# Performance work log

Hardware: AMD Instinct MI355X
Metric: run time of the kernel (lower is better)

Reference implementation:

```python
import jax, jax.numpy as jnp
import numpy as np

N_NODES = 50000
N_EDGES = 400000
N_GRAPHS = 500
N_FEAT = 4
EMB = 200
HID = 128


def setup_inputs() -> dict:
    key = jax.random.key(0)
    ks = jax.random.split(key, 16)
    x = jax.random.normal(ks[0], (N_NODES, N_FEAT), dtype=jnp.float32)
    edge_index = jax.random.randint(ks[1], (2, N_EDGES), 0, N_NODES, dtype=jnp.int64)
    x_scalar = jax.random.normal(ks[2], (N_GRAPHS, N_FEAT), dtype=jnp.float32)
    batch_index = jnp.sort(jax.random.randint(ks[3], (N_NODES,), 0, N_GRAPHS, dtype=jnp.int64))

    def lin(k, fan_in, fan_out):
        return jax.random.normal(k, (fan_in, fan_out), dtype=jnp.float32) / np.sqrt(fan_in)

    params = {
        'W0': lin(ks[4], N_FEAT, EMB), 'b0': jnp.zeros((EMB,), jnp.float32),
        'W1': lin(ks[5], EMB, EMB), 'b1': jnp.zeros((EMB,), jnp.float32),
        'W2': lin(ks[6], EMB, EMB), 'b2': jnp.zeros((EMB,), jnp.float32),
        'W3': lin(ks[7], EMB, EMB), 'b3': jnp.zeros((EMB,), jnp.float32),
        'Wl1': lin(ks[8], EMB + N_FEAT, HID),
        'bl1': jax.random.normal(ks[9], (HID,), jnp.float32) * 0.01,
        'Wl2': lin(ks[10], HID, 1),
        'bl2': jax.random.normal(ks[11], (1,), jnp.float32) * 0.01,
    }
    return dict(x=x, edge_index=edge_index, x_scalar=x_scalar, batch_index=batch_index, **params)


def _gcn_conv(h, W, b, src, dst, norm, num_nodes):
    # PyG GCNConv: h' = D^-1/2 (A+I) D^-1/2 (h W) + b, with precomputed edge norms
    m = (h @ W)[src] * norm[:, None]            # [E+N, out]
    out = jax.ops.segment_sum(m, dst, num_segments=num_nodes)
    return out + b


def reference(x, edge_index, x_scalar, batch_index,
              W0, b0, W1, b1, W2, b2, W3, b3, Wl1, bl1, Wl2, bl2):
    num_nodes = x.shape[0]
    loops = jnp.arange(num_nodes, dtype=edge_index.dtype)
    src = jnp.concatenate([edge_index[0], loops])  # self-loops appended
    dst = jnp.concatenate([edge_index[1], loops])
    deg = jax.ops.segment_sum(jnp.ones_like(dst, dtype=x.dtype), dst, num_segments=num_nodes)
    dinv = deg ** -0.5                              # deg >= 1 due to self-loops
    norm = dinv[src] * dinv[dst]

    h = jax.nn.leaky_relu(_gcn_conv(x, W0, b0, src, dst, norm, num_nodes), 0.01)
    h = jax.nn.leaky_relu(_gcn_conv(h, W1, b1, src, dst, norm, num_nodes), 0.01)
    h = jax.nn.leaky_relu(_gcn_conv(h, W2, b2, src, dst, norm, num_nodes), 0.01)
    h = jax.nn.leaky_relu(_gcn_conv(h, W3, b3, src, dst, norm, num_nodes), 0.01)

    # global mean pool per graph
    sums = jax.ops.segment_sum(h, batch_index, num_segments=N_GRAPHS)
    cnt = jax.ops.segment_sum(jnp.ones((num_nodes,), h.dtype), batch_index, num_segments=N_GRAPHS)
    pooled = sums / jnp.maximum(cnt, 1.0)[:, None]

    g = jnp.concatenate([pooled, x_scalar], axis=1)   # [G, EMB+4]
    g = jax.nn.leaky_relu(g @ Wl1 + bl1, 0.01)
    out = g @ Wl2 + bl2                                # [G, 1]
    return out
```

## Files before the change

kernel.cpp:

```cpp
#include <hip/hip_runtime.h>
#include <math.h>

#define LEAKY(v) ((v) > 0.0f ? (v) : 0.01f * (v))

typedef _Float16 v8h __attribute__((ext_vector_type(8)));
typedef float v4f __attribute__((ext_vector_type(4)));

__global__ void k_count(const int* __restrict__ ei, int* __restrict__ cnt, int E) {
    int e = blockIdx.x * blockDim.x + threadIdx.x;
    if (e < E) atomicAdd(&cnt[ei[E + e]], 1);
}

__global__ __launch_bounds__(256) void k_scan1(const int* __restrict__ cnt,
                                               int* __restrict__ rowptr,
                                               int* __restrict__ bsum, int n) {
    __shared__ int s[256];
    int t = threadIdx.x, i = blockIdx.x * 256 + t;
    int v = (i < n) ? cnt[i] : 0;
    s[t] = v;
    __syncthreads();
    for (int off = 1; off < 256; off <<= 1) {
        int u = (t >= off) ? s[t - off] : 0;
        __syncthreads();
        s[t] += u;
        __syncthreads();
    }
    if (i < n) rowptr[i] = s[t] - v;
    if (t == 255) bsum[blockIdx.x] = s[255];
}

__global__ __launch_bounds__(256) void k_scan2(int* __restrict__ bsum, int nb) {
    __shared__ int s[256];
    int t = threadIdx.x;
    int v = (t < nb) ? bsum[t] : 0;
    s[t] = v;
    __syncthreads();
    for (int off = 1; off < 256; off <<= 1) {
        int u = (t >= off) ? s[t - off] : 0;
        __syncthreads();
        s[t] += u;
        __syncthreads();
    }
    if (t < nb) bsum[t] = s[t] - v;
}

__global__ __launch_bounds__(256) void k_scan3(int* __restrict__ rowptr,
                                               const int* __restrict__ bsum,
                                               const int* __restrict__ cnt,
                                               float* __restrict__ dinv, int n,
                                               float* __restrict__ pooled, int npool) {
    int i = blockIdx.x * 256 + threadIdx.x;
    if (i < n) {
        rowptr[i] += bsum[blockIdx.x];
        dinv[i] = rsqrtf(1.0f + (float)cnt[i]);
    }
    for (int j = i; j < npool; j += gridDim.x * 256) pooled[j] = 0.0f;
}

__global__ void k_fill(const int* __restrict__ ei, const float* __restrict__ dinv,
                       int* __restrict__ rowptr, int2* __restrict__ adj, int E) {
    int e = blockIdx.x * blockDim.x + threadIdx.x;
    if (e < E) {
        int s = ei[e], d = ei[E + e];
        int pos = atomicAdd(&rowptr[d], 1);
        adj[pos] = make_int2(s, __float_as_int(dinv[s] * dinv[d]));
    }
}

__global__ __launch_bounds__(256) void k_splitW3(const float* __restrict__ W1,
                                                 const float* __restrict__ W2,
                                                 const float* __restrict__ W3,
                                                 _Float16* __restrict__ th0, _Float16* __restrict__ tl0,
                                                 _Float16* __restrict__ th1, _Float16* __restrict__ tl1,
                                                 _Float16* __restrict__ th2, _Float16* __restrict__ tl2,
                                                 int* __restrict__ cnt, int n) {
    int layer = blockIdx.y;
    const float* W = (layer == 0) ? W1 : (layer == 1) ? W2 : W3;
    _Float16* Wth = (layer == 0) ? th0 : (layer == 1) ? th1 : th2;
    _Float16* Wtl = (layer == 0) ? tl0 : (layer == 1) ? tl1 : tl2;
    int idx = blockIdx.x * blockDim.x + threadIdx.x;
    int gidx = (blockIdx.y * gridDim.x + blockIdx.x) * 256 + threadIdx.x;
    for (int j = gidx; j < n; j += gridDim.x * gridDim.y * 256) cnt[j] = 0;
    if (idx >= 224 * 208) return;
    int k = idx / 208, c = idx - k * 208;
    float v = (k < 200 && c < 200) ? W[k * 200 + c] : 0.0f;
    _Float16 hi = (_Float16)v;
    _Float16 lo = (_Float16)(v - (float)hi);
    Wth[c * 224 + k] = hi;
    Wtl[c * 224 + k] = lo;
}

__global__ __launch_bounds__(256, 4) void k_gemm200_mfma_l0(const float* __restrict__ x,
                                                            const float* __restrict__ dinv,
                                                            const int* __restrict__ rowptr,
                                                            const int2* __restrict__ adj,
                                                            const float* __restrict__ W0,
                                                            const float* __restrict__ b0,
                                                            const _Float16* __restrict__ Wth,
                                                            const _Float16* __restrict__ Wtl,
                                                            _Float16* __restrict__ T, int M) {
    __shared__ _Float16 Wsh[208 * 32];
    __shared__ _Float16 Wsl[208 * 32];
    __shared__ float W0s[4][200];
    __shared__ float b0s[200];
    const int tid  = threadIdx.x;
    const int lane = tid & 63;
    const int wid  = tid >> 6;
    const int quad = lane >> 4;
    const int l16  = lane & 15;
    const int rowA = blockIdx.x * 64 + wid * 16 + l16;
    const int rowAc = min(rowA, M - 1);

    float w0n = dinv[rowAc]; w0n *= w0n;
    float4 xv = ((const float4*)x)[rowAc];
    float4 pxv = make_float4(xv.x * w0n, xv.y * w0n, xv.z * w0n, xv.w * w0n);
    {
        int lo = rowAc ? rowptr[rowAc - 1] : 0;
        int hi = rowptr[rowAc];
        for (int j = lo; j < hi; ++j) {
            int2 cw = adj[j];
            float w = __int_as_float(cw.y);
            float4 sv = ((const float4*)x)[cw.x];
            pxv.x += sv.x * w; pxv.y += sv.y * w; pxv.z += sv.z * w; pxv.w += sv.w * w;
        }
    }

    for (int idx = tid; idx < 1000; idx += 256) {
        if (idx < 800) W0s[idx / 200][idx % 200] = W0[idx];
        else b0s[idx - 800] = b0[idx - 800];
    }
    __syncthreads();

    v4f acc[13];
#pragma unroll
    for (int t = 0; t < 13; ++t) acc[t] = 0.0f;

    for (int k0 = 0; k0 < 224; k0 += 32) {
        v8h ah, al;
        int kb = k0 + quad * 8;
        if (kb < 200) {
#pragma unroll
            for (int j = 0; j < 8; ++j) {
                int k = kb + j;
                float pv = pxv.x * W0s[0][k] + pxv.y * W0s[1][k]
                         + pxv.z * W0s[2][k] + pxv.w * W0s[3][k] + b0s[k];
                pv = LEAKY(pv);
                _Float16 h = (_Float16)pv;
                ah[j] = h;
                al[j] = (_Float16)(pv - (float)h);
            }
        } else {
#pragma unroll
            for (int j = 0; j < 8; ++j) { ah[j] = (_Float16)0.0f; al[j] = (_Float16)0.0f; }
        }
        __syncthreads();
        for (int idx = tid; idx < 832; idx += 256) {
            int nr = idx >> 2, part = idx & 3;
            *(uint4*)&Wsh[nr * 32 + part * 8] = *(const uint4*)&Wth[nr * 224 + k0 + part * 8];
            *(uint4*)&Wsl[nr * 32 + part * 8] = *(const uint4*)&Wtl[nr * 224 + k0 + part * 8];
        }
        __syncthreads();
#pragma unroll
        for (int t = 0; t < 13; ++t) {
            int nidx = (t * 16 + l16) * 32 + quad * 8;
            v8h wh = *(const v8h*)&Wsh[nidx];
            v8h wl = *(const v8h*)&Wsl[nidx];
            acc[t] = __builtin_amdgcn_mfma_f32_16x16x32_f16(ah, wh, acc[t], 0, 0, 0);
            acc[t] = __builtin_amdgcn_mfma_f32_16x16x32_f16(ah, wl, acc[t], 0, 0, 0);
            acc[t] = __builtin_amdgcn_mfma_f32_16x16x32_f16(al, wh, acc[t], 0, 0, 0);
        }
    }
    const int rb = blockIdx.x * 64 + wid * 16 + quad * 4;
#pragma unroll
    for (int t = 0; t < 13; ++t) {
        int c = t * 16 + l16;
        if (c < 200) {
#pragma unroll
            for (int e = 0; e < 4; ++e) {
                int r = rb + e;
                if (r < M) T[(size_t)r * 200 + c] = (_Float16)acc[t][e];
            }
        }
    }
}

__global__ __launch_bounds__(256, 4) void k_gemm200_mfma(const _Float16* __restrict__ P,
                                                         const float* __restrict__ bias,
                                                         const _Float16* __restrict__ Wth,
                                                         const _Float16* __restrict__ Wtl,
                                                         _Float16* __restrict__ T, int M) {
    __shared__ _Float16 Wsh[208 * 32];
    __shared__ _Float16 Wsl[208 * 32];
    const int tid  = threadIdx.x;
    const int lane = tid & 63;
    const int wid  = tid >> 6;
    const int quad = lane >> 4;
    const int l16  = lane & 15;
    const int rowA = blockIdx.x * 64 + wid * 16 + l16;
    const int rowAc = min(rowA, M - 1);
    const _Float16* Prow = P + (size_t)rowAc * 200;

    v4f acc[13];
#pragma unroll
    for (int t = 0; t < 13; ++t) acc[t] = 0.0f;

    for (int k0 = 0; k0 < 224; k0 += 32) {
        v8h ah, al;
        int kb = k0 + quad * 8;
        if (kb < 200) {
            v8h ph = *(const v8h*)(Prow + kb);
            float4 ba = *(const float4*)(bias + kb);
            float4 bb = *(const float4*)(bias + kb + 4);
            float bv[8] = {ba.x, ba.y, ba.z, ba.w, bb.x, bb.y, bb.z, bb.w};
#pragma unroll
            for (int j = 0; j < 8; ++j) {
                float av = (float)ph[j] + bv[j];
                av = LEAKY(av);
                _Float16 h = (_Float16)av;
                ah[j] = h;
                al[j] = (_Float16)(av - (float)h);
            }
        } else {
#pragma unroll
            for (int j = 0; j < 8; ++j) { ah[j] = (_Float16)0.0f; al[j] = (_Float16)0.0f; }
        }
        __syncthreads();
        for (int idx = tid; idx < 832; idx += 256) {
            int nr = idx >> 2, part = idx & 3;
            *(uint4*)&Wsh[nr * 32 + part * 8] = *(const uint4*)&Wth[nr * 224 + k0 + part * 8];
            *(uint4*)&Wsl[nr * 32 + part * 8] = *(const uint4*)&Wtl[nr * 224 + k0 + part * 8];
        }
        __syncthreads();
#pragma unroll
        for (int t = 0; t < 13; ++t) {
            int nidx = (t * 16 + l16) * 32 + quad * 8;
            v8h wh = *(const v8h*)&Wsh[nidx];
            v8h wl = *(const v8h*)&Wsl[nidx];
            acc[t] = __builtin_amdgcn_mfma_f32_16x16x32_f16(ah, wh, acc[t], 0, 0, 0);
            acc[t] = __builtin_amdgcn_mfma_f32_16x16x32_f16(ah, wl, acc[t], 0, 0, 0);
            acc[t] = __builtin_amdgcn_mfma_f32_16x16x32_f16(al, wh, acc[t], 0, 0, 0);
        }
    }
    const int rb = blockIdx.x * 64 + wid * 16 + quad * 4;
#pragma unroll
    for (int t = 0; t < 13; ++t) {
        int c = t * 16 + l16;
        if (c < 200) {
#pragma unroll
            for (int e = 0; e < 4; ++e) {
                int r = rb + e;
                if (r < M) T[(size_t)r * 200 + c] = (_Float16)acc[t][e];
            }
        }
    }
}

__global__ __launch_bounds__(256) void k_gather200h(const _Float16* __restrict__ t,
                                                    const float* __restrict__ dinv,
                                                    const int* __restrict__ rowptr,
                                                    const int2* __restrict__ adj,
                                                    _Float16* __restrict__ p, int n) {
    int gid = blockIdx.x * blockDim.x + threadIdx.x;
    if (gid >= n * 25) return;
    int v = gid / 25, c8 = gid - v * 25;
    const v8h* tp = (const v8h*)t;
    float w0 = dinv[v]; w0 *= w0;
    v8h tv = tp[v * 25 + c8];
    float a0[8], a1[8];
#pragma unroll
    for (int i = 0; i < 8; ++i) { a0[i] = (float)tv[i] * w0; a1[i] = 0.0f; }
    int lo = v ? rowptr[v - 1] : 0;
    int hi = rowptr[v];
    int j = lo;
    for (; j + 1 < hi; j += 2) {
        int2 e0 = adj[j], e1 = adj[j + 1];
        float wa = __int_as_float(e0.y), wb = __int_as_float(e1.y);
        v8h s0 = tp[e0.x * 25 + c8];
        v8h s1 = tp[e1.x * 25 + c8];
#pragma unroll
        for (int i = 0; i < 8; ++i) {
            a0[i] += (float)s0[i] * wa;
            a1[i] += (float)s1[i] * wb;
        }
    }
    if (j < hi) {
        int2 cw = adj[j];
        float w = __int_as_float(cw.y);
        v8h sv = tp[cw.x * 25 + c8];
#pragma unroll
        for (int i = 0; i < 8; ++i) a0[i] += (float)sv[i] * w;
    }
    v8h o;
#pragma unroll
    for (int i = 0; i < 8; ++i) o[i] = (_Float16)(a0[i] + a1[i]);
    ((v8h*)p)[v * 25 + c8] = o;
}

__global__ __launch_bounds__(256) void k_poolsum(const _Float16* __restrict__ p3,
                                                 const float* __restrict__ b3,
                                                 const int* __restrict__ batch, int n,
                                                 float* __restrict__ pooled) {
    int c = threadIdx.x;
    if (c >= 200) return;
    int base = blockIdx.x * 64;
    int end = min(base + 64, n);
    float bc = b3[c];
    int gprev = batch[base];
    float s = 0.0f;
    for (int i = base; i < end; ++i) {
        int g = batch[i];
        float v = (float)p3[(size_t)i * 200 + c] + bc;
        v = LEAKY(v);
        if (g != gprev) {
            atomicAdd(&pooled[gprev * 200 + c], s);
            s = 0.0f;
            gprev = g;
        }
        s += v;
    }
    atomicAdd(&pooled[gprev * 200 + c], s);
}

__global__ __launch_bounds__(128) void k_mlpfin(const float* __restrict__ pooled,
                                                const int* __restrict__ batch, int n_nodes,
                                                const float* __restrict__ xs,
                                                const float* __restrict__ Wl1,
                                                const float* __restrict__ bl1,
                                                const float* __restrict__ Wl2,
                                                const float* __restrict__ bl2,
                                                float* __restrict__ out) {
    __shared__ float grow[204];
    __shared__ float partial[2];
    __shared__ int sb[2];
    int g = blockIdx.x;
    int t = threadIdx.x;
    if (t == 0) {
        int lo = 0, hi = n_nodes;
        while (lo < hi) { int m = (lo + hi) >> 1; if (batch[m] < g) lo = m + 1; else hi = m; }
        sb[0] = lo;
        int lo2 = lo, hi2 = n_nodes;
        while (lo2 < hi2) { int m = (lo2 + hi2) >> 1; if (batch[m] < g + 1) lo2 = m + 1; else hi2 = m; }
        sb[1] = lo2;
    }
    __syncthreads();
    float inv = 1.0f / fmaxf((float)(sb[1] - sb[0]), 1.0f);
    for (int idx = t; idx < 200; idx += 128) grow[idx] = pooled[g * 200 + idx] * inv;
    if (t < 4) grow[200 + t] = xs[g * 4 + t];
    __syncthreads();
    float s = bl1[t];
    for (int k = 0; k < 204; ++k) s += grow[k] * Wl1[k * 128 + t];
    s = LEAKY(s);
    float hv = s * Wl2[t];
    for (int off = 32; off > 0; off >>= 1) hv += __shfl_down(hv, off, 64);
    if ((t & 63) == 0) partial[t >> 6] = hv;
    __syncthreads();
    if (t == 0) out[g] = partial[0] + partial[1] + bl2[0];
}

extern "C" void kernel_launch(void* const* d_in, const int* in_sizes, int n_in,
                              void* d_out, int out_size, void* d_ws, size_t ws_size,
                              hipStream_t stream) {
    const float* x    = (const float*)d_in[0];
    const int*   ei   = (const int*)d_in[1];
    const float* xs   = (const float*)d_in[2];
    const int*   batch= (const int*)d_in[3];
    const float* W0   = (const float*)d_in[4];
    const float* b0   = (const float*)d_in[5];
    const float* W1   = (const float*)d_in[6];
    const float* b1   = (const float*)d_in[7];
    const float* W2   = (const float*)d_in[8];
    const float* b2   = (const float*)d_in[9];
    const float* W3   = (const float*)d_in[10];
    const float* b3   = (const float*)d_in[11];
    const float* Wl1  = (const float*)d_in[12];
    const float* bl1  = (const float*)d_in[13];
    const float* Wl2  = (const float*)d_in[14];
    const float* bl2  = (const float*)d_in[15];
    float* out = (float*)d_out;

    const int N = in_sizes[0] / 4;
    const int E = in_sizes[1] / 2;
    const int G = in_sizes[2] / 4;

    char* ws = (char*)d_ws;
    size_t off = 0;
    auto alloc = [&](size_t bytes) { void* p = ws + off; off += (bytes + 255) & ~size_t(255); return p; };
    _Float16* bufA = (_Float16*)alloc((size_t)N * 200 * sizeof(_Float16));
    _Float16* bufB = (_Float16*)alloc((size_t)N * 200 * sizeof(_Float16));
    float* dinv   = (float*)alloc((size_t)N * sizeof(float));
    float* pooled = (float*)alloc((size_t)G * 200 * sizeof(float));
    int*   cnt    = (int*)alloc((size_t)N * sizeof(int));
    int*   rowptr = (int*)alloc(((size_t)N + 1) * sizeof(int));
    int*   bsum   = (int*)alloc(256 * sizeof(int));
    int2*  adj    = (int2*)alloc((size_t)E * sizeof(int2));
    _Float16* Wth[3]; _Float16* Wtl[3];
    for (int i = 0; i < 3; ++i) {
        Wth[i] = (_Float16*)alloc(208 * 224 * sizeof(_Float16));
        Wtl[i] = (_Float16*)alloc(208 * 224 * sizeof(_Float16));
    }

    const int B = 256;
    const int nblk = (N + 255) / 256;

    dim3 sg((224 * 208 + B - 1) / B, 3);
    k_splitW3<<<sg, B, 0, stream>>>(W1, W2, W3, Wth[0], Wtl[0], Wth[1], Wtl[1], Wth[2], Wtl[2],
                                    cnt, N);

    k_count<<<(E + B - 1) / B, B, 0, stream>>>(ei, cnt, E);
    k_scan1<<<nblk, 256, 0, stream>>>(cnt, rowptr, bsum, N);
    k_scan2<<<1, 256, 0, stream>>>(bsum, nblk);
    k_scan3<<<nblk, 256, 0, stream>>>(rowptr, bsum, cnt, dinv, N, pooled, G * 200);
    k_fill<<<(E + B - 1) / B, B, 0, stream>>>(ei, dinv, rowptr, adj, E);

    const int gblocks = (N * 25 + 255) / 256;

    k_gemm200_mfma_l0<<<(N + 63) / 64, 256, 0, stream>>>(x, dinv, rowptr, adj, W0, b0,
                                                         Wth[0], Wtl[0], bufA, N);
    k_gather200h<<<gblocks, 256, 0, stream>>>(bufA, dinv, rowptr, adj, bufB, N);

    k_gemm200_mfma<<<(N + 63) / 64, 256, 0, stream>>>(bufB, b1, Wth[1], Wtl[1], bufA, N);
    k_gather200h<<<gblocks, 256, 0, stream>>>(bufA, dinv, rowptr, adj, bufB, N);
    k_gemm200_mfma<<<(N + 63) / 64, 256, 0, stream>>>(bufB, b2, Wth[2], Wtl[2], bufA, N);
    k_gather200h<<<gblocks, 256, 0, stream>>>(bufA, dinv, rowptr, adj, bufB, N);

    k_poolsum<<<(N + 63) / 64, 256, 0, stream>>>(bufB, b3, batch, N, pooled);
    k_mlpfin<<<G, 128, 0, stream>>>(pooled, batch, N, xs, Wl1, bl1, Wl2, bl2, out);
}
```

Before: 359.3 us.

## Fuse neighbor gather into GEMM and final gather into mean-pool kernel

The SpMM gather for layers 1-2 now runs inside the GEMM kernel: each block aggregates its 64 rows into shared memory and then runs the MFMA GEMM from LDS, so the intermediate P buffer never goes to global memory. The last gather is folded into the pooling kernel, which aggregates neighbors per channel before the bias, LeakyReLU and segment sum. This removes three kernel launches and the round trips of the intermediate buffer. The costs are a larger LDS footprint with lower occupancy in the GEMM, and scalar 2-byte per-channel gathers in the pooling kernel instead of 16-byte vector loads.

```diff
diff --git a/kernel.cpp b/kernel.cpp
--- a/kernel.cpp
+++ b/kernel.cpp
@@ -184,11 +184,15 @@
     }
 }
 
-__global__ __launch_bounds__(256, 4) void k_gemm200_mfma(const _Float16* __restrict__ P,
-                                                         const float* __restrict__ bias,
-                                                         const _Float16* __restrict__ Wth,
-                                                         const _Float16* __restrict__ Wtl,
-                                                         _Float16* __restrict__ T, int M) {
+__global__ __launch_bounds__(256, 3) void k_gemm200_fg(const _Float16* __restrict__ T,
+                                                       const float* __restrict__ dinv,
+                                                       const int* __restrict__ rowptr,
+                                                       const int2* __restrict__ adj,
+                                                       const float* __restrict__ bias,
+                                                       const _Float16* __restrict__ Wth,
+                                                       const _Float16* __restrict__ Wtl,
+                                                       _Float16* __restrict__ Out, int M) {
+    __shared__ _Float16 Psh[64][208];
     __shared__ _Float16 Wsh[208 * 32];
     __shared__ _Float16 Wsl[208 * 32];
     const int tid  = threadIdx.x;
@@ -196,9 +200,47 @@
     const int wid  = tid >> 6;
     const int quad = lane >> 4;
     const int l16  = lane & 15;
-    const int rowA = blockIdx.x * 64 + wid * 16 + l16;
-    const int rowAc = min(rowA, M - 1);
-    const _Float16* Prow = P + (size_t)rowAc * 200;
+    const int base = blockIdx.x * 64;
+
+    const v8h* tp = (const v8h*)T;
+    for (int chunk = tid; chunk < 1600; chunk += 256) {
+        int vl = chunk / 25;
+        int c8 = chunk - vl * 25;
+        int v = min(base + vl, M - 1);
+        float w0 = dinv[v]; w0 *= w0;
+        v8h tv = tp[(size_t)v * 25 + c8];
+        float a0[8], a1[8];
+#pragma unroll
+        for (int i = 0; i < 8; ++i) { a0[i] = (float)tv[i] * w0; a1[i] = 0.0f; }
+        int lo = v ? rowptr[v - 1] : 0;
+        int hi = rowptr[v];
+        int j = lo;
+        for (; j + 1 < hi; j += 2) {
+            int2 e0 = adj[j], e1 = adj[j + 1];
+            float wa = __int_as_float(e0.y), wb = __int_as_float(e1.y);
+            v8h s0 = tp[(size_t)e0.x * 25 + c8];
+            v8h s1 = tp[(size_t)e1.x * 25 + c8];
+#pragma unroll
+            for (int i = 0; i < 8; ++i) {
+                a0[i] += (float)s0[i] * wa;
+                a1[i] += (float)s1[i] * wb;
+            }
+        }
+        if (j < hi) {
+            int2 cw = adj[j];
+            float w = __int_as_float(cw.y);
+            v8h sv = tp[(size_t)cw.x * 25 + c8];
+#pragma unroll
+            for (int i = 0; i < 8; ++i) a0[i] += (float)sv[i] * w;
+        }
+        v8h o;
+#pragma unroll
+        for (int i = 0; i < 8; ++i) o[i] = (_Float16)(a0[i] + a1[i]);
+        *(v8h*)&Psh[vl][c8 * 8] = o;
+    }
+    __syncthreads();
+
+    const _Float16* Prow = &Psh[wid * 16 + l16][0];
 
     v4f acc[13];
 #pragma unroll
@@ -241,7 +283,7 @@
             acc[t] = __builtin_amdgcn_mfma_f32_16x16x32_f16(al, wh, acc[t], 0, 0, 0);
         }
     }
-    const int rb = blockIdx.x * 64 + wid * 16 + quad * 4;
+    const int rb = base + wid * 16 + quad * 4;
 #pragma unroll
     for (int t = 0; t < 13; ++t) {
         int c = t * 16 + l16;
@@ -249,67 +291,44 @@
 #pragma unroll
             for (int e = 0; e < 4; ++e) {
                 int r = rb + e;
-                if (r < M) T[(size_t)r * 200 + c] = (_Float16)acc[t][e];
+                if (r < M) Out[(size_t)r * 200 + c] = (_Float16)acc[t][e];
             }
         }
     }
 }
 
-__global__ __launch_bounds__(256) void k_gather200h(const _Float16* __restrict__ t,
+__global__ __launch_bounds__(256) void k_gatherpool(const _Float16* __restrict__ T,
                                                     const float* __restrict__ dinv,
                                                     const int* __restrict__ rowptr,
                                                     const int2* __restrict__ adj,
-                                                    _Float16* __restrict__ p, int n) {
-    int gid = blockIdx.x * blockDim.x + threadIdx.x;
-    if (gid >= n * 25) return;
-    int v = gid / 25, c8 = gid - v * 25;
-    const v8h* tp = (const v8h*)t;
-    float w0 = dinv[v]; w0 *= w0;
-    v8h tv = tp[v * 25 + c8];
-    float a0[8], a1[8];
-#pragma unroll
-    for (int i = 0; i < 8; ++i) { a0[i] = (float)tv[i] * w0; a1[i] = 0.0f; }
-    int lo = v ? rowptr[v - 1] : 0;
-    int hi = rowptr[v];
-    int j = lo;
-    for (; j + 1 < hi; j += 2) {
-        int2 e0 = adj[j], e1 = adj[j + 1];
-        float wa = __int_as_float(e0.y), wb = __int_as_float(e1.y);
-        v8h s0 = tp[e0.x * 25 + c8];
-        v8h s1 = tp[e1.x * 25 + c8];
-#pragma unroll
-        for (int i = 0; i < 8; ++i) {
-            a0[i] += (float)s0[i] * wa;
-            a1[i] += (float)s1[i] * wb;
-        }
-    }
-    if (j < hi) {
-        int2 cw = adj[j];
-        float w = __int_as_float(cw.y);
-        v8h sv = tp[cw.x * 25 + c8];
-#pragma unroll
-        for (int i = 0; i < 8; ++i) a0[i] += (float)sv[i] * w;
-    }
-    v8h o;
-#pragma unroll
-    for (int i = 0; i < 8; ++i) o[i] = (_Float16)(a0[i] + a1[i]);
-    ((v8h*)p)[v * 25 + c8] = o;
-}
-
-__global__ __launch_bounds__(256) void k_poolsum(const _Float16* __restrict__ p3,
-                                                 const float* __restrict__ b3,
-                                                 const int* __restrict__ batch, int n,
-                                                 float* __restrict__ pooled) {
+                                                    const float* __restrict__ b3,
+                                                    const int* __restrict__ batch, int n,
+                                                    float* __restrict__ pooled) {
     int c = threadIdx.x;
     if (c >= 200) return;
-    int base = blockIdx.x * 64;
-    int end = min(base + 64, n);
+    int base = blockIdx.x * 32;
+    int end = min(base + 32, n);
     float bc = b3[c];
     int gprev = batch[base];
     float s = 0.0f;
     for (int i = base; i < end; ++i) {
         int g = batch[i];
-        float v = (float)p3[(size_t)i * 200 + c] + bc;
+        float w0 = dinv[i]; w0 *= w0;
+        float a0 = (float)T[(size_t)i * 200 + c] * w0;
+        float a1 = 0.0f;
+        int lo = i ? rowptr[i - 1] : 0;
+        int hi = rowptr[i];
+        int j = lo;
+        for (; j + 1 < hi; j += 2) {
+            int2 e0 = adj[j], e1 = adj[j + 1];
+            a0 += (float)T[(size_t)e0.x * 200 + c] * __int_as_float(e0.y);
+            a1 += (float)T[(size_t)e1.x * 200 + c] * __int_as_float(e1.y);
+        }
+        if (j < hi) {
+            int2 cw = adj[j];
+            a0 += (float)T[(size_t)cw.x * 200 + c] * __int_as_float(cw.y);
+        }
+        float v = a0 + a1 + bc;
         v = LEAKY(v);
         if (g != gprev) {
             atomicAdd(&pooled[gprev * 200 + c], s);
@@ -412,17 +431,14 @@
     k_scan3<<<nblk, 256, 0, stream>>>(rowptr, bsum, cnt, dinv, N, pooled, G * 200);
     k_fill<<<(E + B - 1) / B, B, 0, stream>>>(ei, dinv, rowptr, adj, E);
 
-    const int gblocks = (N * 25 + 255) / 256;
-
     k_gemm200_mfma_l0<<<(N + 63) / 64, 256, 0, stream>>>(x, dinv, rowptr, adj, W0, b0,
                                                          Wth[0], Wtl[0], bufA, N);
-    k_gather200h<<<gblocks, 256, 0, stream>>>(bufA, dinv, rowptr, adj, bufB, N);
-
-    k_gemm200_mfma<<<(N + 63) / 64, 256, 0, stream>>>(bufB, b1, Wth[1], Wtl[1], bufA, N);
-    k_gather200h<<<gblocks, 256, 0, stream>>>(bufA, dinv, rowptr, adj, bufB, N);
-    k_gemm200_mfma<<<(N + 63) / 64, 256, 0, stream>>>(bufB, b2, Wth[2], Wtl[2], bufA, N);
-    k_gather200h<<<gblocks, 256, 0, stream>>>(bufA, dinv, rowptr, adj, bufB, N);
-
-    k_poolsum<<<(N + 63) / 64, 256, 0, stream>>>(bufB, b3, batch, N, pooled);
+
+    k_gemm200_fg<<<(N + 63) / 64, 256, 0, stream>>>(bufA, dinv, rowptr, adj, b1,
+                                                    Wth[1], Wtl[1], bufB, N);
+    k_gemm200_fg<<<(N + 63) / 64, 256, 0, stream>>>(bufB, dinv, rowptr, adj, b2,
+                                                    Wth[2], Wtl[2], bufA, N);
+
+    k_gatherpool<<<(N + 31) / 32, 256, 0, stream>>>(bufA, dinv, rowptr, adj, b3, batch, N, pooled);
     k_mlpfin<<<G, 128, 0, stream>>>(pooled, batch, N, xs, Wl1, bl1, Wl2, bl2, out);
 }
```

Measured after the change: 438.9 us. +22.1%, slower.

## Pool per graph with binary-search bounds and batch graphs in final MLP

Applied to the files above, without the earlier changes.

Replaces the atomic-based pooling over node chunks with one block per graph. Each block binary-searches its node range and reduces vectorized half-precision rows in shared memory, then writes the mean directly. This removes the pooled zeroing and the float atomics. The final MLP now handles 8 graphs per block and stages Wl1 (about 104KB) in shared memory once per block instead of rereading it per graph. The risk is low occupancy from that large shared allocation and load imbalance across graph sizes.

```diff
diff --git a/kernel.cpp b/kernel.cpp
--- a/kernel.cpp
+++ b/kernel.cpp
@@ -47,14 +47,12 @@
 __global__ __launch_bounds__(256) void k_scan3(int* __restrict__ rowptr,
                                                const int* __restrict__ bsum,
                                                const int* __restrict__ cnt,
-                                               float* __restrict__ dinv, int n,
-                                               float* __restrict__ pooled, int npool) {
+                                               float* __restrict__ dinv, int n) {
     int i = blockIdx.x * 256 + threadIdx.x;
     if (i < n) {
         rowptr[i] += bsum[blockIdx.x];
         dinv[i] = rsqrtf(1.0f + (float)cnt[i]);
     }
-    for (int j = i; j < npool; j += gridDim.x * 256) pooled[j] = 0.0f;
 }
 
 __global__ void k_fill(const int* __restrict__ ei, const float* __restrict__ dinv,
@@ -296,65 +294,84 @@
     ((v8h*)p)[v * 25 + c8] = o;
 }
 
-__global__ __launch_bounds__(256) void k_poolsum(const _Float16* __restrict__ p3,
-                                                 const float* __restrict__ b3,
-                                                 const int* __restrict__ batch, int n,
-                                                 float* __restrict__ pooled) {
-    int c = threadIdx.x;
-    if (c >= 200) return;
-    int base = blockIdx.x * 64;
-    int end = min(base + 64, n);
-    float bc = b3[c];
-    int gprev = batch[base];
-    float s = 0.0f;
-    for (int i = base; i < end; ++i) {
-        int g = batch[i];
-        float v = (float)p3[(size_t)i * 200 + c] + bc;
-        v = LEAKY(v);
-        if (g != gprev) {
-            atomicAdd(&pooled[gprev * 200 + c], s);
-            s = 0.0f;
-            gprev = g;
-        }
-        s += v;
-    }
-    atomicAdd(&pooled[gprev * 200 + c], s);
-}
-
+__global__ __launch_bounds__(256) void k_poolg(const _Float16* __restrict__ T,
+                                               const float* __restrict__ b3,
+                                               const int* __restrict__ batch, int n,
+                                               float* __restrict__ pooled) {
+    __shared__ float part[10][25][9];
+    __shared__ int sb[2];
+    int g = blockIdx.x;
+    int t = threadIdx.x;
+    if (t == 0 || t == 64) {
+        int target = g + (t ? 1 : 0);
+        int lo = 0, hi = n;
+        while (lo < hi) { int m = (lo + hi) >> 1; if (batch[m] < target) lo = m + 1; else hi = m; }
+        sb[t ? 1 : 0] = lo;
+    }
+    __syncthreads();
+    int lo = sb[0], hi = sb[1];
+    int c8 = t % 25, li = t / 25;
+    float acc[8];
+#pragma unroll
+    for (int i = 0; i < 8; ++i) acc[i] = 0.0f;
+    if (li < 10) {
+        const v8h* tp = (const v8h*)T;
+        float4 ba = *(const float4*)(b3 + c8 * 8);
+        float4 bb = *(const float4*)(b3 + c8 * 8 + 4);
+        float bv[8] = {ba.x, ba.y, ba.z, ba.w, bb.x, bb.y, bb.z, bb.w};
+        for (int i = lo + li; i < hi; i += 10) {
+            v8h tv = tp[(size_t)i * 25 + c8];
+#pragma unroll
+            for (int jj = 0; jj < 8; ++jj) {
+                float v = (float)tv[jj] + bv[jj];
+                acc[jj] += LEAKY(v);
+            }
+        }
+#pragma unroll
+        for (int jj = 0; jj < 8; ++jj) part[li][c8][jj] = acc[jj];
+    }
+    __syncthreads();
+    if (t < 200) {
+        int cc8 = t >> 3, jj = t & 7;
+        float s = 0.0f;
+#pragma unroll
+        for (int l2 = 0; l2 < 10; ++l2) s += part[l2][cc8][jj];
+        float inv = 1.0f / fmaxf((float)(hi - lo), 1.0f);
+        pooled[g * 200 + cc8 * 8 + jj] = s * inv;
+    }
+}
+
+#define GPB 8
 __global__ __launch_bounds__(128) void k_mlpfin(const float* __restrict__ pooled,
-                                                const int* __restrict__ batch, int n_nodes,
                                                 const float* __restrict__ xs,
                                                 const float* __restrict__ Wl1,
                                                 const float* __restrict__ bl1,
                                                 const float* __restrict__ Wl2,
                                                 const float* __restrict__ bl2,
-                                                float* __restrict__ out) {
-    __shared__ float grow[204];
+                                                float* __restrict__ out, int G) {
+    __shared__ float Ws[204 * 128];
+    __shared__ float growS[204];
     __shared__ float partial[2];
-    __shared__ int sb[2];
-    int g = blockIdx.x;
     int t = threadIdx.x;
-    if (t == 0) {
-        int lo = 0, hi = n_nodes;
-        while (lo < hi) { int m = (lo + hi) >> 1; if (batch[m] < g) lo = m + 1; else hi = m; }
-        sb[0] = lo;
-        int lo2 = lo, hi2 = n_nodes;
-        while (lo2 < hi2) { int m = (lo2 + hi2) >> 1; if (batch[m] < g + 1) lo2 = m + 1; else hi2 = m; }
-        sb[1] = lo2;
-    }
-    __syncthreads();
-    float inv = 1.0f / fmaxf((float)(sb[1] - sb[0]), 1.0f);
-    for (int idx = t; idx < 200; idx += 128) grow[idx] = pooled[g * 200 + idx] * inv;
-    if (t < 4) grow[200 + t] = xs[g * 4 + t];
-    __syncthreads();
-    float s = bl1[t];
-    for (int k = 0; k < 204; ++k) s += grow[k] * Wl1[k * 128 + t];
-    s = LEAKY(s);
-    float hv = s * Wl2[t];
-    for (int off = 32; off > 0; off >>= 1) hv += __shfl_down(hv, off, 64);
-    if ((t & 63) == 0) partial[t >> 6] = hv;
-    __syncthreads();
-    if (t == 0) out[g] = partial[0] + partial[1] + bl2[0];
+    for (int idx = t; idx < 204 * 128; idx += 128) Ws[idx] = Wl1[idx];
+    float blv = bl1[t], wl2v = Wl2[t], bl2v = bl2[0];
+    int g0 = blockIdx.x * GPB;
+    for (int gi = 0; gi < GPB; ++gi) {
+        int g = g0 + gi;
+        if (g >= G) break;
+        __syncthreads();
+        for (int idx = t; idx < 200; idx += 128) growS[idx] = pooled[g * 200 + idx];
+        if (t < 4) growS[200 + t] = xs[g * 4 + t];
+        __syncthreads();
+        float s = blv;
+        for (int k = 0; k < 204; ++k) s += growS[k] * Ws[k * 128 + t];
+        s = LEAKY(s);
+        float hv = s * wl2v;
+        for (int off = 32; off > 0; off >>= 1) hv += __shfl_down(hv, off, 64);
+        if ((t & 63) == 0) partial[t >> 6] = hv;
+        __syncthreads();
+        if (t == 0) out[g] = partial[0] + partial[1] + bl2v;
+    }
 }
 
 extern "C" void kernel_launch(void* const* d_in, const int* in_sizes, int n_in,
@@ -409,7 +426,7 @@
     k_count<<<(E + B - 1) / B, B, 0, stream>>>(ei, cnt, E);
     k_scan1<<<nblk, 256, 0, stream>>>(cnt, rowptr, bsum, N);
     k_scan2<<<1, 256, 0, stream>>>(bsum, nblk);
-    k_scan3<<<nblk, 256, 0, stream>>>(rowptr, bsum, cnt, dinv, N, pooled, G * 200);
+    k_scan3<<<nblk, 256, 0, stream>>>(rowptr, bsum, cnt, dinv, N);
     k_fill<<<(E + B - 1) / B, B, 0, stream>>>(ei, dinv, rowptr, adj, E);
 
     const int gblocks = (N * 25 + 255) / 256;
@@ -423,6 +440,6 @@
     k_gemm200_mfma<<<(N + 63) / 64, 256, 0, stream>>>(bufB, b2, Wth[2], Wtl[2], bufA, N);
     k_gather200h<<<gblocks, 256, 0, stream>>>(bufA, dinv, rowptr, adj, bufB, N);
 
-    k_poolsum<<<(N + 63) / 64, 256, 0, stream>>>(bufB, b3, batch, N, pooled);
-    k_mlpfin<<<G, 128, 0, stream>>>(pooled, batch, N, xs, Wl1, bl1, Wl2, bl2, out);
-}
+    k_poolg<<<G, 256, 0, stream>>>(bufB, b3, batch, N, pooled);
+    k_mlpfin<<<(G + GPB - 1) / GPB, 128, 0, stream>>>(pooled, xs, Wl1, bl1, Wl2, bl2, out, G);
+}
```

After: 367.2 us. +2.2%, slower.
